# Kernel tuning notes

Measured on AMD Instinct MI355X. Metric: run time of the kernel, lower is better.

Reference implementation:

```python
import jax, jax.numpy as jnp
import numpy as np
import math

EMBED_DIM = 1024
NUM_HEADS = 16
HEAD_DIM = EMBED_DIM // NUM_HEADS
ACT_BITS = 8
WGT_BITS = 8


def fake_quant(x, n_bits):
    # Per-tensor symmetric fake quantization with straight-through estimator.
    qmax = 2.0 ** (n_bits - 1) - 1.0  # 127 for 8 bits
    scale = jnp.maximum(jnp.max(jnp.abs(x)) / qmax, 1e-8)
    q = jnp.clip(jnp.round(x / scale), -qmax - 1.0, qmax) * scale
    return x + jax.lax.stop_gradient(q - x)


def setup_inputs() -> dict:
    key = jax.random.key(0)
    ks = jax.random.split(key, 7)
    S, B, D = 2048, 2, EMBED_DIM
    return {
        "query": jax.random.normal(ks[0], (S, B, D), dtype=jnp.float32),
        "key": jax.random.normal(ks[1], (S, B, D), dtype=jnp.float32),
        "value": jax.random.normal(ks[2], (S, B, D), dtype=jnp.float32),
        "Wi": jax.random.normal(ks[3], (3 * D, D), dtype=jnp.float32) * (1.0 / math.sqrt(D)),
        "bi": jax.random.normal(ks[4], (3 * D,), dtype=jnp.float32) * 0.01,
        "Wo": jax.random.normal(ks[5], (D, D), dtype=jnp.float32) * (1.0 / math.sqrt(D)),
        "bo": jax.random.normal(ks[6], (D,), dtype=jnp.float32) * 0.01,
    }


def reference(query, key, value, Wi, bi, Wo, bo):
    D, H, hd = EMBED_DIM, NUM_HEADS, HEAD_DIM
    len_q, batch, _ = query.shape
    len_k = key.shape[0]

    Wi_q = fake_quant(Wi, WGT_BITS)
    Wo_q = fake_quant(Wo, WGT_BITS)

    # in-projections (full 3D projection per input, then chunk, as in source)
    Xq = fake_quant(query @ Wi_q.T + bi, ACT_BITS)
    Xk = fake_quant(key @ Wi_q.T + bi, ACT_BITS)
    Xv = fake_quant(value @ Wi_q.T + bi, ACT_BITS)
    Q = Xq[..., :D]
    K = Xk[..., D:2 * D]
    V = Xv[..., 2 * D:]

    # [len, B, D] -> [B*H, len, hd]
    q = Q.reshape(len_q, batch * H, hd).transpose(1, 0, 2)
    k = K.reshape(len_k, batch * H, hd).transpose(1, 0, 2)
    v = V.reshape(len_k, batch * H, hd).transpose(1, 0, 2)

    q = fake_quant(q / math.sqrt(hd), ACT_BITS)
    attn = jnp.einsum('bqd,bkd->bqk', q, k)  # note: attn/softmax fake-quants in source are no-ops (result discarded)
    attn = jax.nn.softmax(attn, axis=-1)
    heads = fake_quant(jnp.einsum('bqk,bkd->bqd', attn, v), ACT_BITS)

    # [B*H, len_q, hd] -> [len_q*B, D]
    heads_reshape = heads.transpose(1, 0, 2).reshape(len_q * batch, D)
    y = (heads_reshape @ Wo_q.T + bo).reshape(len_q, batch, D)
    return fake_quant(y, ACT_BITS)
```

## Files before the change

### kernel.cpp

```cpp
#include <hip/hip_runtime.h>
#include <math.h>


typedef _Float16 f16;
typedef _Float16 half8 __attribute__((ext_vector_type(8)));
typedef _Float16 half4 __attribute__((ext_vector_type(4)));
typedef _Float16 half2v __attribute__((ext_vector_type(2)));
typedef __fp16 fp16x2 __attribute__((ext_vector_type(2)));
typedef float floatx4 __attribute__((ext_vector_type(4)));
typedef int int4v __attribute__((ext_vector_type(4)));

#define QMAX 127.0f

#define SLOT_WI 0
#define SLOT_WO 1
#define SLOT_XQ 2
#define SLOT_XK 3
#define SLOT_XV 4
#define SLOT_HD 5
#define SLOT_Y  6
#define SLOT_Q  7
#define SLOT_A  8

__device__ __forceinline__ float slot_scale(const unsigned* slots, int slot, float premul) {
  if (slot < 0) return 1.0f;
  return fmaxf(__uint_as_float(slots[slot]) * premul / QMAX, 1e-8f);
}

__device__ __forceinline__ float slot_scaleA(const unsigned* slots) {
  return fmaxf(__uint_as_float(slots[SLOT_A]) / 16256.0f, 1e-8f);
}

__device__ __forceinline__ void gl2lds16(const void* gsrc, void* ldst) {
  __builtin_amdgcn_global_load_lds((__attribute__((address_space(1))) void*)gsrc,
                                   (__attribute__((address_space(3))) void*)ldst, 16, 0, 0);
}

__device__ __forceinline__ half2v pack2(float a, float b) {
  fp16x2 r = __builtin_amdgcn_cvt_pkrtz(a, b);
  return __builtin_bit_cast(half2v, r);
}

__device__ __forceinline__ size_t swz(int m, int k) {
  return ((size_t)(m >> 4) << 14) + (size_t)(((k >> 6) << 10) +
         (((k >> 4) & 3) << 8) + ((m & 15) << 4) + (k & 15));
}

__global__ __launch_bounds__(64) void init_slots_k(unsigned* slots) {
  if (threadIdx.x < 16) slots[threadIdx.x] = 0u;
}

__global__ __launch_bounds__(256) void absmax3_k(const float* __restrict__ Wi,
                                                 const float* __restrict__ Wo,
                                                 const float* __restrict__ q,
                                                 const float* __restrict__ k,
                                                 const float* __restrict__ v,
                                                 unsigned* __restrict__ slots) {
  __shared__ float red[256];
  int tid = threadIdx.x;
  int bid = blockIdx.x;
  const float4* x4;
  int n4, i0, stride, slot;
  if (bid < 768) {
    x4 = (const float4*)Wi; n4 = 786432; i0 = bid * 256 + tid;
    stride = 768 * 256; slot = SLOT_WI;
  } else if (bid < 1024) {
    x4 = (const float4*)Wo; n4 = 262144; i0 = (bid - 768) * 256 + tid;
    stride = 256 * 256; slot = SLOT_WO;
  } else {
    int r = bid - 1024;
    int t = r >> 9;
    x4 = (const float4*)(t == 0 ? q : (t == 1 ? k : v));
    n4 = 1048576; i0 = (r & 511) * 256 + tid;
    stride = 512 * 256; slot = SLOT_A;
  }
  float lmax = 0.f;
  for (int i = i0; i < n4; i += stride) {
    float4 vv = x4[i];
    lmax = fmaxf(lmax, fmaxf(fmaxf(fabsf(vv.x), fabsf(vv.y)), fmaxf(fabsf(vv.z), fabsf(vv.w))));
  }
  red[tid] = lmax; __syncthreads();
  for (int sh = 128; sh > 0; sh >>= 1) {
    if (tid < sh) red[tid] = fmaxf(red[tid], red[tid + sh]);
    __syncthreads();
  }
  if (tid == 0) atomicMax(&slots[slot], __float_as_uint(red[0]));
}

__global__ __launch_bounds__(256) void quantw_k(const float* __restrict__ Wi,
                                                const float* __restrict__ Wo,
                                                char* __restrict__ Wi8,
                                                char* __restrict__ Wo8,
                                                const unsigned* __restrict__ slots) {
  int tid = threadIdx.x;
  if (blockIdx.x < 768) {
    float s = slot_scale(slots, SLOT_WI, 1.0f);
    const float4* in4 = (const float4*)Wi;
    for (int i = blockIdx.x * 256 + tid; i < 786432; i += 768 * 256) {
      float4 v = in4[i];
      int n = i >> 8, kk = (i & 255) * 4;
      char4 o;
      o.x = (signed char)(int)fminf(fmaxf(rintf(v.x / s), -128.0f), 127.0f);
      o.y = (signed char)(int)fminf(fmaxf(rintf(v.y / s), -128.0f), 127.0f);
      o.z = (signed char)(int)fminf(fmaxf(rintf(v.z / s), -128.0f), 127.0f);
      o.w = (signed char)(int)fminf(fmaxf(rintf(v.w / s), -128.0f), 127.0f);
      *(char4*)(Wi8 + swz(n, kk)) = o;
    }
  } else {
    float s = slot_scale(slots, SLOT_WO, 1.0f);
    const float4* in4 = (const float4*)Wo;
    for (int i = (blockIdx.x - 768) * 256 + tid; i < 262144; i += 256 * 256) {
      float4 v = in4[i];
      int n = i >> 8, kk = (i & 255) * 4;
      char4 o;
      o.x = (signed char)(int)fminf(fmaxf(rintf(v.x / s), -128.0f), 127.0f);
      o.y = (signed char)(int)fminf(fmaxf(rintf(v.y / s), -128.0f), 127.0f);
      o.z = (signed char)(int)fminf(fmaxf(rintf(v.z / s), -128.0f), 127.0f);
      o.w = (signed char)(int)fminf(fmaxf(rintf(v.w / s), -128.0f), 127.0f);
      *(char4*)(Wo8 + swz(n, kk)) = o;
    }
  }
}

__global__ __launch_bounds__(256) void digitize_k(const float* __restrict__ q,
                                                  const float* __restrict__ k,
                                                  const float* __restrict__ v,
                                                  char* __restrict__ A1,
                                                  char* __restrict__ A2,
                                                  const unsigned* __restrict__ slots) {
  float inv = 1.0f / slot_scaleA(slots);
  for (int i = blockIdx.x * 256 + threadIdx.x; i < 3145728; i += gridDim.x * 256) {
    int t = i >> 20;
    int g = i & 1048575;
    const float4* src = (const float4*)(t == 0 ? q : (t == 1 ? k : v));
    float4 x = src[g];
    int m = g >> 8, kk = (g & 255) * 4;
    float xs[4] = {x.x, x.y, x.z, x.w};
    signed char c1s[4], c2s[4];
#pragma unroll
    for (int u = 0; u < 4; ++u) {
      float qv = fminf(fmaxf(rintf(xs[u] * inv), -16256.0f), 16256.0f);
      float c1 = rintf(qv * 0.0078125f);
      c1s[u] = (signed char)(int)c1;
      c2s[u] = (signed char)(int)(qv - 128.0f * c1);
    }
    size_t off = (size_t)t * 4194304 + swz(m, kk);
    *(char4*)(A1 + off) = make_char4(c1s[0], c1s[1], c1s[2], c1s[3]);
    *(char4*)(A2 + off) = make_char4(c2s[0], c2s[1], c2s[2], c2s[3]);
  }
}

__global__ __launch_bounds__(256) void quantf_k(const float* __restrict__ in, float* __restrict__ out,
                                                int n4, unsigned* __restrict__ slots,
                                                int sSlot, float premul) {
  float s = slot_scale(slots, sSlot, premul);
  const float4* in4 = (const float4*)in;
  float4* out4 = (float4*)out;
  for (int i = blockIdx.x * 256 + threadIdx.x; i < n4; i += gridDim.x * 256) {
    float4 v = in4[i];
    float xs[4] = {v.x, v.y, v.z, v.w};
#pragma unroll
    for (int u = 0; u < 4; ++u) {
      float r = rintf((xs[u] * premul) / s);
      r = fminf(fmaxf(r, -128.0f), 127.0f);
      xs[u] = r * s;
    }
    out4[i] = make_float4(xs[0], xs[1], xs[2], xs[3]);
  }
}

__global__ __launch_bounds__(256) void quanti_k(const float* __restrict__ in, f16* __restrict__ out,
                                                int n4, unsigned* __restrict__ slots,
                                                int sSlot, int outAbsSlot) {
  __shared__ float red[256];
  float s = slot_scale(slots, sSlot, 1.0f);
  float lmax = 0.f;
  const float4* in4 = (const float4*)in;
  for (int i = blockIdx.x * 256 + threadIdx.x; i < n4; i += gridDim.x * 256) {
    float4 v = in4[i];
    float xs[4] = {v.x, v.y, v.z, v.w};
    half4 o;
#pragma unroll
    for (int u = 0; u < 4; ++u) {
      float r = rintf(xs[u] / s);
      r = fminf(fmaxf(r, -128.0f), 127.0f);
      o[u] = (f16)r;
      lmax = fmaxf(lmax, fabsf(r));
    }
    *(half4*)(out + (size_t)i * 4) = o;
  }
  if (outAbsSlot >= 0) {
    int tid = threadIdx.x;
    red[tid] = lmax; __syncthreads();
    for (int sh = 128; sh > 0; sh >>= 1) {
      if (tid < sh) red[tid] = fmaxf(red[tid], red[tid + sh]);
      __syncthreads();
    }
    if (tid == 0) atomicMax(&slots[outAbsSlot], __float_as_uint(red[0] * s));
  }
}

__global__ __launch_bounds__(256) void quant8_k(const float* __restrict__ in, char* __restrict__ out,
                                                int n4, const unsigned* __restrict__ slots,
                                                int sSlot) {
  float s = slot_scale(slots, sSlot, 1.0f);
  const float4* in4 = (const float4*)in;
  for (int i = blockIdx.x * 256 + threadIdx.x; i < n4; i += gridDim.x * 256) {
    float4 v = in4[i];
    int m = i >> 8, kk = (i & 255) * 4;
    char4 o;
    o.x = (signed char)(int)fminf(fmaxf(rintf(v.x / s), -128.0f), 127.0f);
    o.y = (signed char)(int)fminf(fmaxf(rintf(v.y / s), -128.0f), 127.0f);
    o.z = (signed char)(int)fminf(fmaxf(rintf(v.z / s), -128.0f), 127.0f);
    o.w = (signed char)(int)fminf(fmaxf(rintf(v.w / s), -128.0f), 127.0f);
    *(char4*)(out + swz(m, kk)) = o;
  }
}

__global__ __launch_bounds__(256) void quantv_t_k(const float* __restrict__ Xv,
                                                  f16* __restrict__ Vt,
                                                  const unsigned* __restrict__ slots) {
  __shared__ f16 T[64][68];
  int tid = threadIdx.x;
  int bh = blockIdx.y, b = bh >> 4, h = bh & 15;
  int k0 = blockIdx.x * 64;
  float s = slot_scale(slots, SLOT_XV, 1.0f);
#pragma unroll
  for (int it = 0; it < 4; ++it) {
    int idx = tid + it * 256;
    int row = idx >> 4, dseg = idx & 15;
    float4 v = *(const float4*)(Xv + ((size_t)(k0 + row) * 2 + b) * 1024 + h * 64 + dseg * 4);
    float xs[4] = {v.x, v.y, v.z, v.w};
    half4 o;
#pragma unroll
    for (int u = 0; u < 4; ++u) {
      float r = rintf(xs[u] / s);
      o[u] = (f16)fminf(fmaxf(r, -128.0f), 127.0f);
    }
    *(half4*)&T[row][dseg * 4] = o;
  }
  __syncthreads();
#pragma unroll
  for (int it = 0; it < 2; ++it) {
    int sdx = tid + it * 256;
    int d = sdx >> 3, j8 = sdx & 7;
    half8 o;
#pragma unroll
    for (int l = 0; l < 8; ++l) {
      int pos = j8 * 8 + l;
      int tp = pos >> 5, pq = (pos & 31) >> 3, jj = pos & 7;
      int k = tp * 32 + pq * 4 + ((jj < 4) ? jj : jj + 12);
      o[l] = T[k][d];
    }
    *(half8*)(Vt + ((size_t)bh * 64 + d) * 2048 + k0 + j8 * 8) = o;
  }
}

__global__ __launch_bounds__(512) void gemm_qkv_i8_k(const char* __restrict__ A1,
                                                     const char* __restrict__ A2,
                                                     const char* __restrict__ B8,
                                                     const float* __restrict__ bias,
                                                     float* __restrict__ Xout,
                                                     unsigned* __restrict__ slots) {
  __shared__ char As1[2][8192];
  __shared__ char As2[2][8192];
  __shared__ char Bs8[2][8192];
  __shared__ float red[512];

  int tid = threadIdx.x;
  int lane = tid & 63, w = tid >> 6;
  int wm = w >> 1, wn = w & 1;
  int quad = lane >> 4, l15 = lane & 15;
  int t = blockIdx.y >> 5;
  int m0 = (blockIdx.y & 31) * 128;
  int n0 = blockIdx.x * 128;
  size_t aoff = (size_t)t * 4194304;

  const char* a1p = A1 + aoff;
  const char* a2p = A2 + aoff;

  int4v acc1[2][4], acc2[2][4];
#pragma unroll
  for (int i = 0; i < 2; ++i)
#pragma unroll
    for (int j = 0; j < 4; ++j) {
      acc1[i][j] = (int4v){0, 0, 0, 0};
      acc2[i][j] = (int4v){0, 0, 0, 0};
    }

  auto stage = [&](int buf, int kk) __attribute__((always_inline)) {
    size_t ac = ((size_t)((m0 >> 4) + w) << 14) + ((kk >> 6) << 10) + lane * 16;
    size_t bc = ((size_t)((n0 >> 4) + w) << 14) + ((kk >> 6) << 10) + lane * 16;
    gl2lds16(a1p + ac, &As1[buf][w * 1024]);
    gl2lds16(a2p + ac, &As2[buf][w * 1024]);
    gl2lds16(B8 + bc, &Bs8[buf][w * 1024]);
  };

  auto compute = [&](int buf) __attribute__((always_inline)) {
    int4v bf[4];
#pragma unroll
    for (int j = 0; j < 4; ++j)
      bf[j] = *(const int4v*)&Bs8[buf][(wn * 4 + j) * 1024 + lane * 16];
    int4v a1f[2];
#pragma unroll
    for (int i = 0; i < 2; ++i)
      a1f[i] = *(const int4v*)&As1[buf][(wm * 2 + i) * 1024 + lane * 16];
#pragma unroll
    for (int i = 0; i < 2; ++i)
#pragma unroll
      for (int j = 0; j < 4; ++j)
        acc1[i][j] = __builtin_amdgcn_mfma_i32_16x16x64_i8(a1f[i], bf[j], acc1[i][j], 0, 0, 0);
    int4v a2f[2];
#pragma unroll
    for (int i = 0; i < 2; ++i)
      a2f[i] = *(const int4v*)&As2[buf][(wm * 2 + i) * 1024 + lane * 16];
#pragma unroll
    for (int i = 0; i < 2; ++i)
#pragma unroll
      for (int j = 0; j < 4; ++j)
        acc2[i][j] = __builtin_amdgcn_mfma_i32_16x16x64_i8(a2f[i], bf[j], acc2[i][j], 0, 0, 0);
  };

  stage(0, 0);
  __syncthreads();
  for (int kt = 0; kt < 7; ++kt) {
    stage(1, (2 * kt + 1) * 64);
    compute(0);
    __syncthreads();
    stage(0, (2 * kt + 2) * 64);
    compute(1);
    __syncthreads();
  }
  stage(1, 960);
  compute(0);
  __syncthreads();
  compute(1);

  float sc = slot_scaleA(slots) * slot_scale(slots, SLOT_WI, 1.0f);
  int colLo = t * 1024;
  float* outT = Xout + aoff;
  float lmax = 0.f;
#pragma unroll
  for (int i = 0; i < 2; ++i) {
#pragma unroll
    for (int j = 0; j < 4; ++j) {
      int gn = n0 + wn * 64 + j * 16 + l15;
      float bv = bias[gn];
      bool wr = (gn >= colLo && gn < colLo + 1024);
#pragma unroll
      for (int r = 0; r < 4; ++r) {
        int gm = m0 + wm * 32 + i * 16 + quad * 4 + r;
        float vv = fmaf((float)acc1[i][j][r], 128.0f, (float)acc2[i][j][r]) * sc + bv;
        lmax = fmaxf(lmax, fabsf(vv));
        if (wr) outT[(size_t)gm * 1024 + (gn - colLo)] = vv;
      }
    }
  }
  red[tid] = lmax; __syncthreads();
  for (int sh = 256; sh > 0; sh >>= 1) {
    if (tid < sh) red[tid] = fmaxf(red[tid], red[tid + sh]);
    __syncthreads();
  }
  if (tid == 0) atomicMax(&slots[SLOT_XQ + t], __float_as_uint(red[0]));
}

__global__ __launch_bounds__(512) void gemm_i8out_k(const char* __restrict__ A8,
                                                    const char* __restrict__ B8,
                                                    const float* __restrict__ bias,
                                                    float* __restrict__ out,
                                                    unsigned* __restrict__ slots) {
  __shared__ char As8[2][8192];
  __shared__ char Bs8[2][8192];
  __shared__ float red[512];

  int tid = threadIdx.x;
  int lane = tid & 63, w = tid >> 6;
  int wm = w >> 1, wn = w & 1;
  int quad = lane >> 4, l15 = lane & 15;
  int m0 = blockIdx.y * 128, n0 = blockIdx.x * 128;

  int4v acc[2][4];
#pragma unroll
  for (int i = 0; i < 2; ++i)
#pragma unroll
    for (int j = 0; j < 4; ++j) acc[i][j] = (int4v){0, 0, 0, 0};

  auto stage = [&](int buf, int kk) __attribute__((always_inline)) {
    size_t ac = ((size_t)((m0 >> 4) + w) << 14) + ((kk >> 6) << 10) + lane * 16;
    size_t bc = ((size_t)((n0 >> 4) + w) << 14) + ((kk >> 6) << 10) + lane * 16;
    gl2lds16(A8 + ac, &As8[buf][w * 1024]);
    gl2lds16(B8 + bc, &Bs8[buf][w * 1024]);
  };

  auto compute = [&](int buf) __attribute__((always_inline)) {
    int4v bf[4];
#pragma unroll
    for (int j = 0; j < 4; ++j)
      bf[j] = *(const int4v*)&Bs8[buf][(wn * 4 + j) * 1024 + lane * 16];
    int4v af[2];
#pragma unroll
    for (int i = 0; i < 2; ++i)
      af[i] = *(const int4v*)&As8[buf][(wm * 2 + i) * 1024 + lane * 16];
#pragma unroll
    for (int i = 0; i < 2; ++i)
#pragma unroll
      for (int j = 0; j < 4; ++j)
        acc[i][j] = __builtin_amdgcn_mfma_i32_16x16x64_i8(af[i], bf[j], acc[i][j], 0, 0, 0);
  };

  stage(0, 0);
  __syncthreads();
  for (int kt = 0; kt < 7; ++kt) {
    stage(1, (2 * kt + 1) * 64);
    compute(0);
    __syncthreads();
    stage(0, (2 * kt + 2) * 64);
    compute(1);
    __syncthreads();
  }
  stage(1, 960);
  compute(0);
  __syncthreads();
  compute(1);

  float sc = slot_scale(slots, SLOT_HD, 1.0f) * slot_scale(slots, SLOT_WO, 1.0f);
  float lmax = 0.f;
#pragma unroll
  for (int i = 0; i < 2; ++i) {
#pragma unroll
    for (int j = 0; j < 4; ++j) {
      int gn = n0 + wn * 64 + j * 16 + l15;
      float bv = bias[gn];
#pragma unroll
      for (int r = 0; r < 4; ++r) {
        int gm = m0 + wm * 32 + i * 16 + quad * 4 + r;
        float v = (float)acc[i][j][r] * sc + bv;
        lmax = fmaxf(lmax, fabsf(v));
        out[(size_t)gm * 1024 + gn] = v;
      }
    }
  }
  red[tid] = lmax; __syncthreads();
  for (int sh = 256; sh > 0; sh >>= 1) {
    if (tid < sh) red[tid] = fmaxf(red[tid], red[tid + sh]);
    __syncthreads();
  }
  if (tid == 0) atomicMax(&slots[SLOT_Y], __float_as_uint(red[0]));
}

__global__ __launch_bounds__(256) void attn_k(const f16* __restrict__ Qc,
                                              const f16* __restrict__ Kh,
                                              const f16* __restrict__ Vt,
                                              float* __restrict__ heads,
                                              unsigned* __restrict__ slots) {
  __shared__ f16 Ks[64 * 64];
  __shared__ f16 Vs[64][72];
  __shared__ float lred[4][2][16];
  __shared__ float red[256];

  int tid = threadIdx.x;
  int lane = tid & 63, w = tid >> 6;
  int quad = lane >> 4, l15 = lane & 15;
  int bh = blockIdx.y, b = bh >> 4, h = bh & 15;
  int q0 = blockIdx.x * 128;

  float s1 = slot_scale(slots, SLOT_XQ, 1.0f);
  float sq = slot_scale(slots, SLOT_Q, 0.125f);
  float sk = slot_scale(slots, SLOT_XK, 1.0f);
  float sv = slot_scale(slots, SLOT_XV, 1.0f);
  float cS = sq * sk * 1.44269504088896340736f;
  const float FOFF = 12.0f;

  half8 qf[2][2];
#pragma unroll
  for (int s = 0; s < 2; ++s) {
    const f16* qrow = Qc + ((size_t)(q0 + w * 32 + s * 16 + l15) * 2 + b) * 1024 + h * 64;
    half8 qr0 = *(const half8*)(qrow + quad * 8);
    half8 qr1 = *(const half8*)(qrow + 32 + quad * 8);
#pragma unroll
    for (int u = 0; u < 8; ++u) {
      float x0 = ((float)qr0[u] * s1) * 0.125f;
      float x1 = ((float)qr1[u] * s1) * 0.125f;
      qf[s][0][u] = (f16)fminf(fmaxf(rintf(x0 / sq), -128.0f), 127.0f);
      qf[s][1][u] = (f16)fminf(fmaxf(rintf(x1 / sq), -128.0f), 127.0f);
    }
  }

  int ksrow = lane >> 3;
  int ksp = lane & 7;
  int vr0 = tid >> 3, vs0 = (tid & 7) * 8;

  floatx4 oacc[2][4];
#pragma unroll
  for (int s = 0; s < 2; ++s)
#pragma unroll
    for (int d = 0; d < 4; ++d) oacc[s][d] = (floatx4){0.f, 0.f, 0.f, 0.f};
  float lsum[2] = {0.f, 0.f};

  const f16* vbase = Vt + (size_t)bh * 131072;

  for (int kt = 0; kt < 2048; kt += 64) {
    __syncthreads();
#pragma unroll
    for (int t = 0; t < 2; ++t) {
      int r0 = (w * 2 + t) * 8;
      int row = r0 + ksrow;
      int g = ksp ^ (row & 7);
      gl2lds16(Kh + ((size_t)(kt + row) * 2 + b) * 1024 + h * 64 + g * 8, &Ks[r0 * 64]);
    }
    half8 va = *(const half8*)(vbase + (size_t)vr0 * 2048 + kt + vs0);
    half8 vb = *(const half8*)(vbase + (size_t)(vr0 + 32) * 2048 + kt + vs0);
    *(half8*)&Vs[vr0][vs0] = va;
    *(half8*)&Vs[vr0 + 32][vs0] = vb;
    __syncthreads();

    half8 aph[2][2], apl[2][2];
#pragma unroll
    for (int t = 0; t < 4; ++t) {
      int row = t * 16 + l15;
      int g1 = quad ^ (row & 7);
      half8 kf0 = *(half8*)&Ks[row * 64 + g1 * 8];
      half8 kf1 = *(half8*)&Ks[row * 64 + (g1 ^ 4) * 8];
      int tp = t >> 1, hi = (t & 1) * 4;
#pragma unroll
      for (int s = 0; s < 2; ++s) {
        floatx4 sacc = (floatx4){0.f, 0.f, 0.f, 0.f};
        sacc = __builtin_amdgcn_mfma_f32_16x16x32_f16(kf0, qf[s][0], sacc, 0, 0, 0);
        sacc = __builtin_amdgcn_mfma_f32_16x16x32_f16(kf1, qf[s][1], sacc, 0, 0, 0);
        float p0 = __builtin_amdgcn_exp2f(fmaf(sacc[0], cS, -FOFF));
        float p1 = __builtin_amdgcn_exp2f(fmaf(sacc[1], cS, -FOFF));
        float p2 = __builtin_amdgcn_exp2f(fmaf(sacc[2], cS, -FOFF));
        float p3 = __builtin_amdgcn_exp2f(fmaf(sacc[3], cS, -FOFF));
        lsum[s] += (p0 + p1) + (p2 + p3);
        half2v h01 = pack2(p0, p1);
        half2v h23 = pack2(p2, p3);
        half2v l01 = pack2(p0 - (float)h01[0], p1 - (float)h01[1]);
        half2v l23 = pack2(p2 - (float)h23[0], p3 - (float)h23[1]);
        aph[s][tp][hi + 0] = h01[0]; aph[s][tp][hi + 1] = h01[1];
        aph[s][tp][hi + 2] = h23[0]; aph[s][tp][hi + 3] = h23[1];
        apl[s][tp][hi + 0] = l01[0]; apl[s][tp][hi + 1] = l01[1];
        apl[s][tp][hi + 2] = l23[0]; apl[s][tp][hi + 3] = l23[1];
      }
    }

#pragma unroll
    for (int d = 0; d < 4; ++d) {
      const f16* vsrow = &Vs[d * 16 + l15][0];
      half8 b0 = *(const half8*)(vsrow + quad * 8);
      half8 b1 = *(const half8*)(vsrow + 32 + quad * 8);
#pragma unroll
      for (int s = 0; s < 2; ++s) {
        oacc[s][d] = __builtin_amdgcn_mfma_f32_16x16x32_f16(aph[s][0], b0, oacc[s][d], 0, 0, 0);
        oacc[s][d] = __builtin_amdgcn_mfma_f32_16x16x32_f16(apl[s][0], b0, oacc[s][d], 0, 0, 0);
        oacc[s][d] = __builtin_amdgcn_mfma_f32_16x16x32_f16(aph[s][1], b1, oacc[s][d], 0, 0, 0);
        oacc[s][d] = __builtin_amdgcn_mfma_f32_16x16x32_f16(apl[s][1], b1, oacc[s][d], 0, 0, 0);
      }
    }
  }

#pragma unroll
  for (int s = 0; s < 2; ++s) {
    float l = lsum[s];
    l += __shfl_xor(l, 16);
    l += __shfl_xor(l, 32);
    lred[w][s][l15] = l;
  }
  float linv[2][4];
#pragma unroll
  for (int s = 0; s < 2; ++s)
#pragma unroll
    for (int r = 0; r < 4; ++r) linv[s][r] = sv / lred[w][s][quad * 4 + r];

  float lmax = 0.f;
#pragma unroll
  for (int s = 0; s < 2; ++s)
#pragma unroll
    for (int d = 0; d < 4; ++d)
#pragma unroll
      for (int r = 0; r < 4; ++r) {
        float hv = oacc[s][d][r] * linv[s][r];
        heads[((size_t)(q0 + w * 32 + s * 16 + quad * 4 + r) * 2 + b) * 1024 +
              h * 64 + d * 16 + l15] = hv;
        lmax = fmaxf(lmax, fabsf(hv));
      }
  red[tid] = lmax; __syncthreads();
  for (int sh = 128; sh > 0; sh >>= 1) {
    if (tid < sh) red[tid] = fmaxf(red[tid], red[tid + sh]);
    __syncthreads();
  }
  if (tid == 0) atomicMax(&slots[SLOT_HD], __float_as_uint(red[0]));
}

extern "C" void kernel_launch(void* const* d_in, const int* in_sizes, int n_in,
                              void* d_out, int out_size, void* d_ws, size_t ws_size,
                              hipStream_t stream) {
  (void)in_sizes; (void)n_in; (void)out_size; (void)ws_size;
  const float* query = (const float*)d_in[0];
  const float* key   = (const float*)d_in[1];
  const float* value = (const float*)d_in[2];
  const float* Wi    = (const float*)d_in[3];
  const float* bi    = (const float*)d_in[4];
  const float* Wo    = (const float*)d_in[5];
  const float* bo    = (const float*)d_in[6];
  float* out = (float*)d_out;

  char* p = (char*)d_ws;
  unsigned* slots = (unsigned*)p;            p += 1024;
  char* Wi8 = p;                             p += 3072 * 1024;
  char* Wo8 = p;                             p += 1024 * 1024;
  char* A1  = p;                             p += 12288 * 1024;
  char* A2  = p;                             p += 12288 * 1024;
  float* Hd = (float*)A1;
  f16* Kint = (f16*)(A2 + 4194304);
  float* Xq = (float*)p;                     p += 4096 * 1024 * 4;
  float* Y  = Xq;
  float* Xk = (float*)p;                     p += 4096 * 1024 * 4;
  f16* Qc   = (f16*)Xk;
  float* Xv = (float*)p;                     p += 4096 * 1024 * 4;
  char* Hint8 = (char*)Xv + 4096 * 1024 * 2;
  f16* Vt   = (f16*)p;                       p += 4096 * 1024 * 2;

  init_slots_k<<<1, 64, 0, stream>>>(slots);
  absmax3_k<<<2560, 256, 0, stream>>>(Wi, Wo, query, key, value, slots);
  quantw_k<<<1024, 256, 0, stream>>>(Wi, Wo, Wi8, Wo8, slots);
  digitize_k<<<2048, 256, 0, stream>>>(query, key, value, A1, A2, slots);

  dim3 gq(24, 96);
  gemm_qkv_i8_k<<<gq, 512, 0, stream>>>(A1, A2, Wi8, bi, Xq, slots);

  quanti_k<<<1024, 256, 0, stream>>>(Xk, Kint, 1048576, slots, SLOT_XK, -1);
  quanti_k<<<1024, 256, 0, stream>>>(Xq, Qc, 1048576, slots, SLOT_XQ, SLOT_Q);

  dim3 gvt(32, 32);
  quantv_t_k<<<gvt, 256, 0, stream>>>(Xv, Vt, slots);

  dim3 ga(16, 32);
  attn_k<<<ga, 256, 0, stream>>>(Qc, Kint, Vt, Hd, slots);

  quant8_k<<<1024, 256, 0, stream>>>(Hd, Hint8, 1048576, slots, SLOT_HD);

  dim3 g2(8, 32);
  gemm_i8out_k<<<g2, 512, 0, stream>>>(Hint8, Wo8, bo, Y, slots);

  quantf_k<<<1024, 256, 0, stream>>>(Y, out, 1048576, slots, SLOT_Y, 1.0f);
}
```

Baseline: 381.9 us.

## Write swizzled int8 tiles with 16-byte stores and fuse Q/K quantization launches

The quantize/digitize kernels now assign each thread one 16-byte swizzled output chunk. Each thread gathers the matching 16 contiguous floats from a row and writes a single int4 store, replacing scattered char4 stores. The two quanti launches are merged into one kernel, init_slots becomes hipMemsetAsync, and GEMM reduction buffers alias the A-tile shared memory to cut LDS use. The aim is fewer small uncoalesced writes and fewer launches. The cost is per-thread loads that stride across rows, and relying on the alias being safe after the main loop.

```diff
diff --git a/kernel.cpp b/kernel.cpp
--- a/kernel.cpp
+++ b/kernel.cpp
@@ -41,14 +41,6 @@
   return __builtin_bit_cast(half2v, r);
 }
 
-__device__ __forceinline__ size_t swz(int m, int k) {
-  return ((size_t)(m >> 4) << 14) + (size_t)(((k >> 6) << 10) +
-         (((k >> 4) & 3) << 8) + ((m & 15) << 4) + (k & 15));
-}
-
-__global__ __launch_bounds__(64) void init_slots_k(unsigned* slots) {
-  if (threadIdx.x < 16) slots[threadIdx.x] = 0u;
-}
 
 __global__ __launch_bounds__(256) void absmax3_k(const float* __restrict__ Wi,
                                                  const float* __restrict__ Wo,
@@ -92,34 +84,26 @@
                                                 char* __restrict__ Wi8,
                                                 char* __restrict__ Wo8,
                                                 const unsigned* __restrict__ slots) {
-  int tid = threadIdx.x;
-  if (blockIdx.x < 768) {
-    float s = slot_scale(slots, SLOT_WI, 1.0f);
-    const float4* in4 = (const float4*)Wi;
-    for (int i = blockIdx.x * 256 + tid; i < 786432; i += 768 * 256) {
-      float4 v = in4[i];
-      int n = i >> 8, kk = (i & 255) * 4;
-      char4 o;
-      o.x = (signed char)(int)fminf(fmaxf(rintf(v.x / s), -128.0f), 127.0f);
-      o.y = (signed char)(int)fminf(fmaxf(rintf(v.y / s), -128.0f), 127.0f);
-      o.z = (signed char)(int)fminf(fmaxf(rintf(v.z / s), -128.0f), 127.0f);
-      o.w = (signed char)(int)fminf(fmaxf(rintf(v.w / s), -128.0f), 127.0f);
-      *(char4*)(Wi8 + swz(n, kk)) = o;
-    }
+  int j = blockIdx.x * 256 + threadIdx.x;
+  const float* src; char* dst; float s; int a;
+  if (j < 196608) {
+    s = slot_scale(slots, SLOT_WI, 1.0f); src = Wi; dst = Wi8; a = j;
   } else {
-    float s = slot_scale(slots, SLOT_WO, 1.0f);
-    const float4* in4 = (const float4*)Wo;
-    for (int i = (blockIdx.x - 768) * 256 + tid; i < 262144; i += 256 * 256) {
-      float4 v = in4[i];
-      int n = i >> 8, kk = (i & 255) * 4;
-      char4 o;
-      o.x = (signed char)(int)fminf(fmaxf(rintf(v.x / s), -128.0f), 127.0f);
-      o.y = (signed char)(int)fminf(fmaxf(rintf(v.y / s), -128.0f), 127.0f);
-      o.z = (signed char)(int)fminf(fmaxf(rintf(v.z / s), -128.0f), 127.0f);
-      o.w = (signed char)(int)fminf(fmaxf(rintf(v.w / s), -128.0f), 127.0f);
-      *(char4*)(Wo8 + swz(n, kk)) = o;
-    }
-  }
+    s = slot_scale(slots, SLOT_WO, 1.0f); src = Wo; dst = Wo8; a = j - 196608;
+  }
+  int m = ((a >> 10) << 4) | (a & 15);
+  int k0 = ((((a >> 6) & 15) << 2) | ((a >> 4) & 3)) << 4;
+  const float4* row = (const float4*)(src + (size_t)m * 1024 + k0);
+  char ob[16] __attribute__((aligned(16)));
+#pragma unroll
+  for (int c = 0; c < 4; ++c) {
+    float4 x = row[c];
+    float xs[4] = {x.x, x.y, x.z, x.w};
+#pragma unroll
+    for (int u = 0; u < 4; ++u)
+      ob[c * 4 + u] = (signed char)(int)fminf(fmaxf(rintf(xs[u] / s), -128.0f), 127.0f);
+  }
+  *(int4*)(dst + (size_t)a * 16) = *(const int4*)ob;
 }
 
 __global__ __launch_bounds__(256) void digitize_k(const float* __restrict__ q,
@@ -129,25 +113,30 @@
                                                   char* __restrict__ A2,
                                                   const unsigned* __restrict__ slots) {
   float inv = 1.0f / slot_scaleA(slots);
-  for (int i = blockIdx.x * 256 + threadIdx.x; i < 3145728; i += gridDim.x * 256) {
-    int t = i >> 20;
-    int g = i & 1048575;
-    const float4* src = (const float4*)(t == 0 ? q : (t == 1 ? k : v));
-    float4 x = src[g];
-    int m = g >> 8, kk = (g & 255) * 4;
+  int j = blockIdx.x * 256 + threadIdx.x;
+  int t = j >> 18;
+  int a = j & 262143;
+  const float* src = (t == 0 ? q : (t == 1 ? k : v));
+  int m = ((a >> 10) << 4) | (a & 15);
+  int k0 = ((((a >> 6) & 15) << 2) | ((a >> 4) & 3)) << 4;
+  const float4* row = (const float4*)(src + (size_t)m * 1024 + k0);
+  char o1[16] __attribute__((aligned(16)));
+  char o2[16] __attribute__((aligned(16)));
+#pragma unroll
+  for (int c = 0; c < 4; ++c) {
+    float4 x = row[c];
     float xs[4] = {x.x, x.y, x.z, x.w};
-    signed char c1s[4], c2s[4];
 #pragma unroll
     for (int u = 0; u < 4; ++u) {
       float qv = fminf(fmaxf(rintf(xs[u] * inv), -16256.0f), 16256.0f);
       float c1 = rintf(qv * 0.0078125f);
-      c1s[u] = (signed char)(int)c1;
-      c2s[u] = (signed char)(int)(qv - 128.0f * c1);
-    }
-    size_t off = (size_t)t * 4194304 + swz(m, kk);
-    *(char4*)(A1 + off) = make_char4(c1s[0], c1s[1], c1s[2], c1s[3]);
-    *(char4*)(A2 + off) = make_char4(c2s[0], c2s[1], c2s[2], c2s[3]);
-  }
+      o1[c * 4 + u] = (signed char)(int)c1;
+      o2[c * 4 + u] = (signed char)(int)(qv - 128.0f * c1);
+    }
+  }
+  size_t off = (size_t)t * 4194304 + (size_t)a * 16;
+  *(int4*)(A1 + off) = *(const int4*)o1;
+  *(int4*)(A2 + off) = *(const int4*)o2;
 }
 
 __global__ __launch_bounds__(256) void quantf_k(const float* __restrict__ in, float* __restrict__ out,
@@ -169,14 +158,20 @@
   }
 }
 
-__global__ __launch_bounds__(256) void quanti_k(const float* __restrict__ in, f16* __restrict__ out,
-                                                int n4, unsigned* __restrict__ slots,
-                                                int sSlot, int outAbsSlot) {
+__global__ __launch_bounds__(256) void quanti2_k(const float* __restrict__ Xk,
+                                                 f16* __restrict__ Kint,
+                                                 const float* __restrict__ Xq,
+                                                 f16* __restrict__ Qc,
+                                                 unsigned* __restrict__ slots) {
   __shared__ float red[256];
-  float s = slot_scale(slots, sSlot, 1.0f);
+  bool isQ = blockIdx.x >= 1024;
+  const float* in = isQ ? Xq : Xk;
+  f16* out = isQ ? Qc : Kint;
+  float s = slot_scale(slots, isQ ? SLOT_XQ : SLOT_XK, 1.0f);
+  int b = isQ ? blockIdx.x - 1024 : blockIdx.x;
   float lmax = 0.f;
   const float4* in4 = (const float4*)in;
-  for (int i = blockIdx.x * 256 + threadIdx.x; i < n4; i += gridDim.x * 256) {
+  for (int i = b * 256 + threadIdx.x; i < 1048576; i += 1024 * 256) {
     float4 v = in4[i];
     float xs[4] = {v.x, v.y, v.z, v.w};
     half4 o;
@@ -189,32 +184,35 @@
     }
     *(half4*)(out + (size_t)i * 4) = o;
   }
-  if (outAbsSlot >= 0) {
+  if (isQ) {
     int tid = threadIdx.x;
     red[tid] = lmax; __syncthreads();
     for (int sh = 128; sh > 0; sh >>= 1) {
       if (tid < sh) red[tid] = fmaxf(red[tid], red[tid + sh]);
       __syncthreads();
     }
-    if (tid == 0) atomicMax(&slots[outAbsSlot], __float_as_uint(red[0] * s));
+    if (tid == 0) atomicMax(&slots[SLOT_Q], __float_as_uint(red[0] * s));
   }
 }
 
 __global__ __launch_bounds__(256) void quant8_k(const float* __restrict__ in, char* __restrict__ out,
-                                                int n4, const unsigned* __restrict__ slots,
+                                                const unsigned* __restrict__ slots,
                                                 int sSlot) {
   float s = slot_scale(slots, sSlot, 1.0f);
-  const float4* in4 = (const float4*)in;
-  for (int i = blockIdx.x * 256 + threadIdx.x; i < n4; i += gridDim.x * 256) {
-    float4 v = in4[i];
-    int m = i >> 8, kk = (i & 255) * 4;
-    char4 o;
-    o.x = (signed char)(int)fminf(fmaxf(rintf(v.x / s), -128.0f), 127.0f);
-    o.y = (signed char)(int)fminf(fmaxf(rintf(v.y / s), -128.0f), 127.0f);
-    o.z = (signed char)(int)fminf(fmaxf(rintf(v.z / s), -128.0f), 127.0f);
-    o.w = (signed char)(int)fminf(fmaxf(rintf(v.w / s), -128.0f), 127.0f);
-    *(char4*)(out + swz(m, kk)) = o;
-  }
+  int a = blockIdx.x * 256 + threadIdx.x;
+  int m = ((a >> 10) << 4) | (a & 15);
+  int k0 = ((((a >> 6) & 15) << 2) | ((a >> 4) & 3)) << 4;
+  const float4* row = (const float4*)(in + (size_t)m * 1024 + k0);
+  char ob[16] __attribute__((aligned(16)));
+#pragma unroll
+  for (int c = 0; c < 4; ++c) {
+    float4 x = row[c];
+    float xs[4] = {x.x, x.y, x.z, x.w};
+#pragma unroll
+    for (int u = 0; u < 4; ++u)
+      ob[c * 4 + u] = (signed char)(int)fminf(fmaxf(rintf(xs[u] / s), -128.0f), 127.0f);
+  }
+  *(int4*)(out + (size_t)a * 16) = *(const int4*)ob;
 }
 
 __global__ __launch_bounds__(256) void quantv_t_k(const float* __restrict__ Xv,
@@ -265,7 +263,7 @@
   __shared__ char As1[2][8192];
   __shared__ char As2[2][8192];
   __shared__ char Bs8[2][8192];
-  __shared__ float red[512];
+  float* red = (float*)&As1[0][0];
 
   int tid = threadIdx.x;
   int lane = tid & 63, w = tid >> 6;
@@ -371,7 +369,7 @@
                                                     unsigned* __restrict__ slots) {
   __shared__ char As8[2][8192];
   __shared__ char Bs8[2][8192];
-  __shared__ float red[512];
+  float* red = (float*)&As8[0][0];
 
   int tid = threadIdx.x;
   int lane = tid & 63, w = tid >> 6;
@@ -620,16 +618,15 @@
   char* Hint8 = (char*)Xv + 4096 * 1024 * 2;
   f16* Vt   = (f16*)p;                       p += 4096 * 1024 * 2;
 
-  init_slots_k<<<1, 64, 0, stream>>>(slots);
+  hipMemsetAsync(slots, 0, 64, stream);
   absmax3_k<<<2560, 256, 0, stream>>>(Wi, Wo, query, key, value, slots);
   quantw_k<<<1024, 256, 0, stream>>>(Wi, Wo, Wi8, Wo8, slots);
-  digitize_k<<<2048, 256, 0, stream>>>(query, key, value, A1, A2, slots);
+  digitize_k<<<3072, 256, 0, stream>>>(query, key, value, A1, A2, slots);
 
   dim3 gq(24, 96);
   gemm_qkv_i8_k<<<gq, 512, 0, stream>>>(A1, A2, Wi8, bi, Xq, slots);
 
-  quanti_k<<<1024, 256, 0, stream>>>(Xk, Kint, 1048576, slots, SLOT_XK, -1);
-  quanti_k<<<1024, 256, 0, stream>>>(Xq, Qc, 1048576, slots, SLOT_XQ, SLOT_Q);
+  quanti2_k<<<2048, 256, 0, stream>>>(Xk, Kint, Xq, Qc, slots);
 
   dim3 gvt(32, 32);
   quantv_t_k<<<gvt, 256, 0, stream>>>(Xv, Vt, slots);
@@ -637,7 +634,7 @@
   dim3 ga(16, 32);
   attn_k<<<ga, 256, 0, stream>>>(Qc, Kint, Vt, Hd, slots);
 
-  quant8_k<<<1024, 256, 0, stream>>>(Hd, Hint8, 1048576, slots, SLOT_HD);
+  quant8_k<<<1024, 256, 0, stream>>>(Hd, Hint8, slots, SLOT_HD);
 
   dim3 g2(8, 32);
   gemm_i8out_k<<<g2, 512, 0, stream>>>(Hint8, Wo8, bo, Y, slots);
```

Measured after the change: 375.9 us. No clear change (-1.6%).
